# Kernel tuning notes

Hardware: AMD Instinct MI355X
Metric: run time of the kernel (lower is better)

Reference implementation:

```python
import jax, jax.numpy as jnp
import numpy as np

KERNEL_SIZE = 3
PAD = (KERNEL_SIZE - 1) // 2  # =1, 'same' padding for stride=1, dilation=1


def setup_inputs() -> dict:
    key = jax.random.key(0)
    k1, k2, k3, k4 = jax.random.split(key, 4)
    bs, h, w = 8, 352, 1216
    kk = KERNEL_SIZE * KERNEL_SIZE
    return {
        "kernel": jax.random.normal(k1, (bs, kk, h, w), dtype=jnp.float32),
        "iter_weight": jax.random.uniform(k2, (1,), dtype=jnp.float32),
        "input": jax.random.normal(k3, (bs, 1, h, w), dtype=jnp.float32),
        "input0": jax.random.normal(k4, (bs, 1, h, w), dtype=jnp.float32),
    }


def reference(kernel, iter_weight, input, input0):
    bs, _, h, w = input.shape
    kk = KERNEL_SIZE * KERNEL_SIZE
    mid = (kk - 1) // 2  # center tap index (4 for 3x3)

    # im2col / F.unfold for a single channel: stack the k*k shifted views.
    xp = jnp.pad(input[:, 0], ((0, 0), (PAD, PAD), (PAD, PAD)))
    patches = jnp.stack(
        [xp[:, i:i + h, j:j + w] for i in range(KERNEL_SIZE) for j in range(KERNEL_SIZE)],
        axis=1,
    )  # (bs, k*k, h, w), same tap ordering as F.unfold

    # Replace the center tap with the original (sparse) depth input0.
    patches = patches.at[:, mid].set(input0[:, 0])

    # Per-pixel weighted sum over the k*k taps: einsum('ijk,ijk->ik') in torch.
    kernel = kernel.reshape(bs, kk, h, w)
    cspn_output = jnp.einsum("bkhw,bkhw->bhw", patches, kernel).reshape(bs, 1, h, w)

    # NOTE: the torch module computes `output = iter_weight * cspn_output + input`
    # but returns cspn_output; we match that (iter_weight does not affect output).
    return cspn_output
```

## Files before the change

kernel.cpp:

```cpp
#include <hip/hip_runtime.h>


#define BS 8
#define H  352
#define W  1216
#define HW (H * W)

__global__ __launch_bounds__(256) void cspn_kernel(
    const float* __restrict__ kern,
    const float* __restrict__ in,
    const float* __restrict__ in0,
    float* __restrict__ out)
{
    const int groupsPerImg = HW / 4;
    const int total = BS * groupsPerImg;
    int idx = blockIdx.x * blockDim.x + threadIdx.x;
    if (idx >= total) return;

    int b   = idx / groupsPerImg;
    int rem = idx - b * groupsPerImg;
    int h   = rem / (W / 4);
    int wg  = rem - h * (W / 4);
    int w0  = wg * 4;

    const float* inb  = in  + (size_t)b * HW;
    const float* in0b = in0 + (size_t)b * HW;
    const float* kb   = kern + ((size_t)b * 9) * HW + (size_t)h * W + w0;

    float4 acc = {0.f, 0.f, 0.f, 0.f};

    #pragma unroll
    for (int di = -1; di <= 1; ++di) {
        int hh = h + di;
        if (hh < 0 || hh >= H) continue;

        const float* row = inb + (size_t)hh * W + w0;
        float4 x   = *(const float4*)row;
        float  xm1 = (w0 > 0)     ? row[-1] : 0.f;
        float  xp4 = (w0 + 4 < W) ? row[4]  : 0.f;

        float4 c = x;
        if (di == 0) c = *(const float4*)(in0b + (size_t)h * W + w0);

        float4 l = {xm1, x.x, x.y, x.z};
        float4 r = {x.y, x.z, x.w, xp4};

        int t = (di + 1) * 3;
        float4 k0 = *(const float4*)(kb + (size_t)t       * HW);
        float4 k1 = *(const float4*)(kb + (size_t)(t + 1) * HW);
        float4 k2 = *(const float4*)(kb + (size_t)(t + 2) * HW);

        acc.x += l.x * k0.x + c.x * k1.x + r.x * k2.x;
        acc.y += l.y * k0.y + c.y * k1.y + r.y * k2.y;
        acc.z += l.z * k0.z + c.z * k1.z + r.z * k2.z;
        acc.w += l.w * k0.w + c.w * k1.w + r.w * k2.w;
    }

    *(float4*)(out + (size_t)b * HW + (size_t)h * W + w0) = acc;
}

extern "C" void kernel_launch(void* const* d_in, const int* in_sizes, int n_in,
                              void* d_out, int out_size, void* d_ws, size_t ws_size,
                              hipStream_t stream) {
    const float* kern = (const float*)d_in[0];
    const float* in   = (const float*)d_in[2];
    const float* in0  = (const float*)d_in[3];
    float* out        = (float*)d_out;

    const int total  = BS * (HW / 4);
    const int block  = 256;
    const int grid   = (total + block - 1) / block;
    cspn_kernel<<<grid, block, 0, stream>>>(kern, in, in0, out);
}
```

Measured before the change: 201.1 us.

## Process 8 pixels per thread with nontemporal loads, branchless borders

Each thread now computes 8 output pixels instead of 4, loads all nine kernel taps up front with nontemporal loads, and writes output with nontemporal stores. Border handling uses clamped offsets and multiplicative masks instead of branches, so all loads are issued unconditionally. The goal is more memory-level parallelism and less cache pollution from the large streamed kernel tensor, at the cost of higher register use and half as many threads.

```diff
diff --git a/kernel.cpp b/kernel.cpp
--- a/kernel.cpp
+++ b/kernel.cpp
@@ -5,6 +5,13 @@
 #define H  352
 #define W  1216
 #define HW (H * W)
+#define WG (W / 8)
+
+typedef float vf4 __attribute__((ext_vector_type(4)));
+
+__device__ __forceinline__ vf4 ldnt4(const float* p) {
+    return __builtin_nontemporal_load((const vf4*)p);
+}
 
 __global__ __launch_bounds__(256) void cspn_kernel(
     const float* __restrict__ kern,
@@ -12,51 +19,72 @@
     const float* __restrict__ in0,
     float* __restrict__ out)
 {
-    const int groupsPerImg = HW / 4;
-    const int total = BS * groupsPerImg;
+    const int total = BS * H * WG;
     int idx = blockIdx.x * blockDim.x + threadIdx.x;
     if (idx >= total) return;
 
-    int b   = idx / groupsPerImg;
-    int rem = idx - b * groupsPerImg;
-    int h   = rem / (W / 4);
-    int wg  = rem - h * (W / 4);
-    int w0  = wg * 4;
+    int b   = idx / (H * WG);
+    int rem = idx - b * (H * WG);
+    int h   = rem / WG;
+    int w0  = (rem - h * WG) * 8;
 
-    const float* inb  = in  + (size_t)b * HW;
-    const float* in0b = in0 + (size_t)b * HW;
-    const float* kb   = kern + ((size_t)b * 9) * HW + (size_t)h * W + w0;
+    const float* __restrict__ rowc = in  + (size_t)b * HW + (size_t)h * W + w0;
+    const float* __restrict__ zp   = in0 + (size_t)b * HW + (size_t)h * W + w0;
+    const float* __restrict__ kb   = kern + (size_t)b * 9 * HW + (size_t)h * W + w0;
 
-    float4 acc = {0.f, 0.f, 0.f, 0.f};
+    const float mT = (h > 0)      ? 1.f : 0.f;
+    const float mB = (h < H - 1)  ? 1.f : 0.f;
+    const ptrdiff_t oT = (h > 0)     ? -(ptrdiff_t)W : 0;
+    const ptrdiff_t oB = (h < H - 1) ?  (ptrdiff_t)W : 0;
+    const int   oL = (w0 > 0)     ? -1 : 0;
+    const int   oR = (w0 + 8 < W) ?  8 : 7;
+    const float mL = (w0 > 0)     ? 1.f : 0.f;
+    const float mR = (w0 + 8 < W) ? 1.f : 0.f;
 
+    const float* rowt = rowc + oT;
+    const float* rowb = rowc + oB;
+
+    vf4 t0 = *(const vf4*)(rowt);
+    vf4 t1 = *(const vf4*)(rowt + 4);
+    float tl = rowt[oL], tr = rowt[oR];
+    vf4 c0 = *(const vf4*)(rowc);
+    vf4 c1 = *(const vf4*)(rowc + 4);
+    float cl = rowc[oL], cr = rowc[oR];
+    vf4 bb0 = *(const vf4*)(rowb);
+    vf4 bb1 = *(const vf4*)(rowb + 4);
+    float bl = rowb[oL], br = rowb[oR];
+    vf4 z0 = *(const vf4*)(zp);
+    vf4 z1 = *(const vf4*)(zp + 4);
+
+    float kk[9][8];
     #pragma unroll
-    for (int di = -1; di <= 1; ++di) {
-        int hh = h + di;
-        if (hh < 0 || hh >= H) continue;
-
-        const float* row = inb + (size_t)hh * W + w0;
-        float4 x   = *(const float4*)row;
-        float  xm1 = (w0 > 0)     ? row[-1] : 0.f;
-        float  xp4 = (w0 + 4 < W) ? row[4]  : 0.f;
-
-        float4 c = x;
-        if (di == 0) c = *(const float4*)(in0b + (size_t)h * W + w0);
-
-        float4 l = {xm1, x.x, x.y, x.z};
-        float4 r = {x.y, x.z, x.w, xp4};
-
-        int t = (di + 1) * 3;
-        float4 k0 = *(const float4*)(kb + (size_t)t       * HW);
-        float4 k1 = *(const float4*)(kb + (size_t)(t + 1) * HW);
-        float4 k2 = *(const float4*)(kb + (size_t)(t + 2) * HW);
-
-        acc.x += l.x * k0.x + c.x * k1.x + r.x * k2.x;
-        acc.y += l.y * k0.y + c.y * k1.y + r.y * k2.y;
-        acc.z += l.z * k0.z + c.z * k1.z + r.z * k2.z;
-        acc.w += l.w * k0.w + c.w * k1.w + r.w * k2.w;
+    for (int t = 0; t < 9; ++t) {
+        vf4 ka = ldnt4(kb + (size_t)t * HW);
+        vf4 kc = ldnt4(kb + (size_t)t * HW + 4);
+        kk[t][0] = ka.x; kk[t][1] = ka.y; kk[t][2] = ka.z; kk[t][3] = ka.w;
+        kk[t][4] = kc.x; kk[t][5] = kc.y; kk[t][6] = kc.z; kk[t][7] = kc.w;
     }
 
-    *(float4*)(out + (size_t)b * HW + (size_t)h * W + w0) = acc;
+    float vt[10] = {tl * mL, t0.x, t0.y, t0.z, t0.w, t1.x, t1.y, t1.z, t1.w, tr * mR};
+    float vc[10] = {cl * mL, c0.x, c0.y, c0.z, c0.w, c1.x, c1.y, c1.z, c1.w, cr * mR};
+    float vb[10] = {bl * mL, bb0.x, bb0.y, bb0.z, bb0.w, bb1.x, bb1.y, bb1.z, bb1.w, br * mR};
+    float vz[8]  = {z0.x, z0.y, z0.z, z0.w, z1.x, z1.y, z1.z, z1.w};
+    #pragma unroll
+    for (int i = 0; i < 10; ++i) { vt[i] *= mT; vb[i] *= mB; }
+
+    float acc[8];
+    #pragma unroll
+    for (int i = 0; i < 8; ++i) {
+        acc[i]  = vt[i] * kk[0][i] + vt[i+1] * kk[1][i] + vt[i+2] * kk[2][i];
+        acc[i] += vc[i] * kk[3][i] + vz[i]   * kk[4][i] + vc[i+2] * kk[5][i];
+        acc[i] += vb[i] * kk[6][i] + vb[i+1] * kk[7][i] + vb[i+2] * kk[8][i];
+    }
+
+    float* op = out + (size_t)b * HW + (size_t)h * W + w0;
+    vf4 o0 = {acc[0], acc[1], acc[2], acc[3]};
+    vf4 o1 = {acc[4], acc[5], acc[6], acc[7]};
+    __builtin_nontemporal_store(o0, (vf4*)op);
+    __builtin_nontemporal_store(o1, (vf4*)(op + 4));
 }
 
 extern "C" void kernel_launch(void* const* d_in, const int* in_sizes, int n_in,
@@ -67,8 +95,8 @@
     const float* in0  = (const float*)d_in[3];
     float* out        = (float*)d_out;
 
-    const int total  = BS * (HW / 4);
-    const int block  = 256;
-    const int grid   = (total + block - 1) / block;
+    const int total = BS * H * WG;
+    const int block = 256;
+    const int grid  = (total + block - 1) / block;
     cspn_kernel<<<grid, block, 0, stream>>>(kern, in, in0, out);
 }
```

New measurement: 206.5 us. 1.03x slower.
